# Optimization experiments

Measured on AMD Instinct MI355X. Metric: run time of the kernel, lower is better.

## Reference

```python
import jax, jax.numpy as jnp
import numpy as np

B, D, C, P = 1024, 768, 150, 64  # batch, in_feats, num_labels, proj2 dim
POS_M, NEG_M = 0.7, 1.4


def setup_inputs() -> dict:
    key = jax.random.key(0)
    ks = jax.random.split(key, 8)
    return {
        "x": jax.random.normal(ks[0], (B, D), jnp.float32),
        "lb": jax.random.randint(ks[1], (B,), 0, C + 1),
        "mem": jax.random.normal(ks[2], (C, D), jnp.float32),
        "fc_w": jax.random.normal(ks[3], (2 * D, 2 * D), jnp.float32) * 0.02,
        "fc_b": jnp.zeros((2 * D,), jnp.float32),
        "p1_w": jax.random.normal(ks[4], (1, 2 * D), jnp.float32) * 0.02,
        "p1_b": jnp.zeros((1,), jnp.float32),
        "p2_w": jax.random.normal(ks[5], (P, 2 * D), jnp.float32) * 0.02,
        "p2_b": jnp.zeros((P,), jnp.float32),
    }


def reference(x, lb, mem, fc_w, fc_b, p1_w, p1_b, p2_w, p2_b):
    d = x.shape[1]
    # cat([a, b], 1) @ fc_w.T == a @ Wx.T + b @ Wm.T  (exact split of the linear)
    Wx, Wm = fc_w[:, :d], fc_w[:, d:]
    xh = x @ Wx.T + fc_b                                # [B, 2D]

    # --- get_logit ---
    seen_h = jax.nn.relu(xh[:, None, :] + mem @ Wm.T)   # [B, C, 2D]
    seen = jnp.einsum('bce,e->bc', seen_h, p1_w[0]) + p1_b[0]   # [B, C]
    uh = jax.nn.relu(xh)                                # cat([x, zeros]) path
    unseen = uh @ p1_w.T + p1_b                         # [B, 1]
    logits = jnp.concatenate([seen, unseen], axis=1)    # [B, C+1]

    # --- masked log-softmax losses (pos_adapte) ---
    labels = jax.nn.one_hot(lb, C + 1, dtype=jnp.float32)
    th = jnp.zeros_like(labels).at[:, -1].set(1.0)
    labels = labels.at[:, -1].set(0.0)
    p_mask = labels + th
    n_mask = 1.0 - labels
    BIG = 1e30
    loss1 = -(jax.nn.log_softmax(logits - (1.0 - p_mask) * BIG, -1) * labels).sum(1)
    loss2 = -(jax.nn.log_softmax(logits - (1.0 - n_mask) * BIG, -1) * th).sum(1)
    loss_cls = (loss1 + loss2).mean()

    # --- metric loss on unseen embedding ---
    u = uh @ p2_w.T + p2_b                              # [B, 64]
    u = u / jnp.maximum(jnp.linalg.norm(u, axis=1, keepdims=True), 1e-12)
    sq_n = (u * u).sum(1)
    sq = sq_n[:, None] + sq_n[None, :] - 2.0 * (u @ u.T)
    err = sq <= 0.0
    dist = jnp.sqrt(jnp.clip(sq, 1e-16, None)) * (~err).astype(u.dtype)
    same = lb[:, None] == lb[None, :]
    eye = jnp.eye(dist.shape[0], dtype=bool)
    pos = (same & ~eye).astype(dist.dtype)
    neg = (~same).astype(dist.dtype)
    pos_l = (jax.nn.relu(dist - POS_M) * pos).sum() / jnp.maximum(pos.sum(), 1.0)
    neg_l = (jax.nn.relu(NEG_M - dist) * neg).sum() / jnp.maximum(neg.sum(), 1.0)

    return loss_cls + pos_l + neg_l
```

## Files before the change

kernel.cpp:

```cpp
#include <hip/hip_runtime.h>
#include <math.h>

#define B_    1024
#define D_    768
#define C_    150
#define P_    64
#define TWOD  1536
#define NCLS  151
#define CPAD  256

#define ECHUNKS 16
#define ECHUNK  96
#define ESTEP   32

#define ASTR  40
#define USTRU 120

#define USTR  72

#define OFF_MH      0
#define OFF_XH      (OFF_MH + C_ * TWOD)
#define OFF_PARTIAL (OFF_XH + B_ * TWOD)
#define OFF_UBF     (OFF_PARTIAL + ECHUNKS * B_ * CPAD)
#define OFF_SQN     (OFF_UBF + (B_ * P_) / 2)
#define OFF_CLS     (OFF_SQN + B_)
#define OFF_PAIR    (OFF_CLS + B_)
#define OFF_XBF     (OFF_PAIR + 1024)
#define OFF_MEMBF   (OFF_XBF + (B_ * D_) / 2)
#define OFF_WBF     (OFF_MEMBF + (C_ * D_) / 2)
#define OFF_P2BF    (OFF_WBF + (TWOD * TWOD) / 2)

typedef __bf16 bfx8 __attribute__((ext_vector_type(8)));
typedef float  f32x4 __attribute__((ext_vector_type(4)));

__device__ inline ushort f2bf(float f) {
    union { float f; unsigned u; } c; c.f = f;
    unsigned r = c.u + 0x7fffu + ((c.u >> 16) & 1u);
    return (ushort)(r >> 16);
}

#define X4   (B_ * D_ / 4)
#define MEM4 (C_ * D_ / 4)
#define W4   (TWOD * TWOD / 4)
#define P24  (P_ * TWOD / 4)
#define TOT4 (X4 + MEM4 + W4 + P24)

__global__ __launch_bounds__(256) void prep_bf16(
    const float* __restrict__ x, const float* __restrict__ mem,
    const float* __restrict__ w, const float* __restrict__ p2w,
    ushort* __restrict__ xb, ushort* __restrict__ memb,
    ushort* __restrict__ wb, ushort* __restrict__ p2b)
{
    int i = blockIdx.x * 256 + threadIdx.x;
    if (i >= TOT4) return;
    const float* src; ushort* dst; int off;
    if (i < X4)                  { src = x;   dst = xb;   off = i; }
    else if (i < X4 + MEM4)      { src = mem; dst = memb; off = i - X4; }
    else if (i < X4 + MEM4 + W4) { src = w;   dst = wb;   off = i - X4 - MEM4; }
    else                         { src = p2w; dst = p2b;  off = i - X4 - MEM4 - W4; }
    float4 v = ((const float4*)src)[off];
    ushort4 o;
    o.x = f2bf(v.x); o.y = f2bf(v.y); o.z = f2bf(v.z); o.w = f2bf(v.w);
    ((ushort4*)dst)[off] = o;
}

__global__ __launch_bounds__(256) void gemm_all(
    const ushort* __restrict__ xbf, const ushort* __restrict__ membf,
    const ushort* __restrict__ wbf, const float* __restrict__ fc_b,
    float* __restrict__ xh, float* __restrict__ mh)
{
    __shared__ ushort As[64 * ASTR];
    __shared__ ushort Bs[128 * ASTR];
    const int id = blockIdx.x;
    const int t  = threadIdx.x;

    const ushort* A; float* Out; int M, m0, n0, koff; bool xblk;
    if (id < 192) {
        xblk = true;  A = xbf;  Out = xh; M = B_;
        m0 = (id & 15) * 64; n0 = (id >> 4) * 128; koff = 0;
    } else {
        int q = id - 192;
        xblk = false; A = membf; Out = mh; M = C_;
        m0 = (q % 3) * 64; n0 = (q / 3) * 128; koff = D_;
    }

    const int wave = t >> 6, lane = t & 63;
    const int wm = (wave & 1) * 32, wn = (wave >> 1) * 64;
    const int fm = lane & 15, quad = lane >> 4;

    const int row_a = t >> 2, qa = (t & 3) * 8;
    const int ar = min(m0 + row_a, M - 1);
    const ushort* Arow = A + (size_t)ar * D_ + qa;
    const ushort* Brow = wbf + (size_t)(n0 + row_a) * TWOD + koff + qa;

    f32x4 acc[2][4];
#pragma unroll
    for (int j = 0; j < 4; ++j) {
        float bv = xblk ? fc_b[n0 + wn + j * 16 + fm] : 0.f;
#pragma unroll
        for (int i = 0; i < 2; ++i)
            acc[i][j] = (f32x4){bv, bv, bv, bv};
    }

    uint4 pa  = *(const uint4*)(Arow);
    uint4 pb0 = *(const uint4*)(Brow);
    uint4 pb1 = *(const uint4*)(Brow + 64 * TWOD);

    for (int k0 = 0; k0 < D_; k0 += 32) {
        __syncthreads();
        *(uint4*)&As[row_a * ASTR + qa] = pa;
        *(uint4*)&Bs[row_a * ASTR + qa] = pb0;
        *(uint4*)&Bs[(64 + row_a) * ASTR + qa] = pb1;
        __syncthreads();
        if (k0 + 32 < D_) {
            pa  = *(const uint4*)(Arow + k0 + 32);
            pb0 = *(const uint4*)(Brow + k0 + 32);
            pb1 = *(const uint4*)(Brow + 64 * TWOD + k0 + 32);
        }
        bfx8 af[2], bf[4];
#pragma unroll
        for (int i = 0; i < 2; ++i)
            af[i] = *(const bfx8*)&As[(wm + i * 16 + fm) * ASTR + quad * 8];
#pragma unroll
        for (int j = 0; j < 4; ++j)
            bf[j] = *(const bfx8*)&Bs[(wn + j * 16 + fm) * ASTR + quad * 8];
#pragma unroll
        for (int i = 0; i < 2; ++i)
#pragma unroll
            for (int j = 0; j < 4; ++j)
                acc[i][j] = __builtin_amdgcn_mfma_f32_16x16x32_bf16(
                    af[i], bf[j], acc[i][j], 0, 0, 0);
    }

#pragma unroll
    for (int i = 0; i < 2; ++i)
#pragma unroll
        for (int j = 0; j < 4; ++j)
#pragma unroll
            for (int r = 0; r < 4; ++r) {
                int row = m0 + wm + i * 16 + quad * 4 + r;
                int col = n0 + wn + j * 16 + fm;
                if (row < M) Out[(size_t)row * TWOD + col] = acc[i][j][r];
            }
}

__global__ __launch_bounds__(256) void fused_tile(
    const float* __restrict__ xh, const float* __restrict__ mh,
    const float* __restrict__ p1w, const ushort* __restrict__ p2bf,
    float* __restrict__ partial)
{
    __shared__ __align__(16) char smem[46080];
    const int t  = threadIdx.x;
    const int b0 = blockIdx.x * 128;
    const int z  = blockIdx.z;

    if (blockIdx.y == 3) {
        ushort* Au = (ushort*)smem;
        ushort* Wu = (ushort*)(smem + 128 * USTRU * 2);
        const int kb = z * ECHUNK;
        const int wave = t >> 6, lane = t & 63;
        const int fm = lane & 15, quad = lane >> 4;

        {
            const int row = t >> 1, kh = (t & 1) * 48;
            const float* xr_ = xh + (size_t)(b0 + row) * TWOD + kb + kh;
            ushort tmp[48];
#pragma unroll
            for (int i = 0; i < 12; ++i) {
                float4 v = *(const float4*)&xr_[i * 4];
                tmp[i * 4 + 0] = f2bf(fmaxf(v.x, 0.f));
                tmp[i * 4 + 1] = f2bf(fmaxf(v.y, 0.f));
                tmp[i * 4 + 2] = f2bf(fmaxf(v.z, 0.f));
                tmp[i * 4 + 3] = f2bf(fmaxf(v.w, 0.f));
            }
#pragma unroll
            for (int i = 0; i < 6; ++i)
                *(uint4*)&Au[row * USTRU + kh + i * 8] = *(const uint4*)&tmp[i * 8];
        }
        {
            const int row = t >> 2, ks = (t & 3) * 24;
            const ushort* pw = p2bf + (size_t)row * TWOD + kb + ks;
#pragma unroll
            for (int i = 0; i < 3; ++i)
                *(uint4*)&Wu[row * USTRU + ks + i * 8] = *(const uint4*)&pw[i * 8];
        }
        __syncthreads();

        f32x4 uacc[2][4];
#pragma unroll
        for (int i = 0; i < 2; ++i)
#pragma unroll
            for (int j = 0; j < 4; ++j) uacc[i][j] = (f32x4){0.f, 0.f, 0.f, 0.f};
#pragma unroll
        for (int k0 = 0; k0 < ECHUNK; k0 += 32) {
            bfx8 af[2], bf[4];
#pragma unroll
            for (int i = 0; i < 2; ++i)
                af[i] = *(const bfx8*)&Au[(wave * 32 + i * 16 + fm) * USTRU + k0 + quad * 8];
#pragma unroll
            for (int j = 0; j < 4; ++j)
                bf[j] = *(const bfx8*)&Wu[(j * 16 + fm) * USTRU + k0 + quad * 8];
#pragma unroll
            for (int i = 0; i < 2; ++i)
#pragma unroll
                for (int j = 0; j < 4; ++j)
                    uacc[i][j] = __builtin_amdgcn_mfma_f32_16x16x32_bf16(
                        af[i], bf[j], uacc[i][j], 0, 0, 0);
        }
#pragma unroll
        for (int i = 0; i < 2; ++i)
#pragma unroll
            for (int j = 0; j < 4; ++j)
#pragma unroll
                for (int r = 0; r < 4; ++r) {
                    int row = b0 + wave * 32 + i * 16 + quad * 4 + r;
                    partial[((size_t)z * B_ + row) * CPAD + 192 + j * 16 + fm] =
                        uacc[i][j][r];
                }
        return;
    }

    float* xT  = (float*)smem;
    float* mT  = (float*)(smem + ESTEP * 128 * 4);
    float* wT1 = (float*)(smem + ESTEP * 192 * 4);

    const int c0 = blockIdx.y * 64;
    const int e0 = z * ECHUNK;
    const int tm = t & 15;
    const int tn = t >> 4;

    const int xr = t & 127, xh16 = (t >> 7) * 16;
    const int mc = t & 63,  mq8 = ((t >> 6) & 3) * 8;
    const int gc = c0 + mc;
    const bool cseen = gc < C_;
    const float* xrow = xh + (size_t)(b0 + xr) * TWOD;
    const float* mrow = mh + (size_t)(cseen ? gc : 0) * TWOD;

    float acc[8][4] = {};

    for (int es = 0; es < ECHUNK; es += ESTEP) {
        const int eb = e0 + es;
        float4 xv[4];
#pragma unroll
        for (int i = 0; i < 4; ++i)
            xv[i] = *(const float4*)&xrow[eb + xh16 + i * 4];
        float4 mv0 = cseen ? *(const float4*)&mrow[eb + mq8]
                           : make_float4(0.f, 0.f, 0.f, 0.f);
        float4 mv1 = cseen ? *(const float4*)&mrow[eb + mq8 + 4]
                           : make_float4(0.f, 0.f, 0.f, 0.f);
        float4 wv = (t < 8) ? *(const float4*)&p1w[eb + t * 4]
                            : make_float4(0.f, 0.f, 0.f, 0.f);
        __syncthreads();
#pragma unroll
        for (int i = 0; i < 4; ++i) {
            xT[(xh16 + i * 4 + 0) * 128 + xr] = xv[i].x;
            xT[(xh16 + i * 4 + 1) * 128 + xr] = xv[i].y;
            xT[(xh16 + i * 4 + 2) * 128 + xr] = xv[i].z;
            xT[(xh16 + i * 4 + 3) * 128 + xr] = xv[i].w;
        }
        mT[(mq8 + 0) * 64 + mc] = mv0.x; mT[(mq8 + 1) * 64 + mc] = mv0.y;
        mT[(mq8 + 2) * 64 + mc] = mv0.z; mT[(mq8 + 3) * 64 + mc] = mv0.w;
        mT[(mq8 + 4) * 64 + mc] = mv1.x; mT[(mq8 + 5) * 64 + mc] = mv1.y;
        mT[(mq8 + 6) * 64 + mc] = mv1.z; mT[(mq8 + 7) * 64 + mc] = mv1.w;
        if (t < 8) *(float4*)&wT1[t * 4] = wv;
        __syncthreads();

#pragma unroll 4
        for (int e = 0; e < ESTEP; ++e) {
            float a[8], m[4];
            *(float4*)&a[0] = *(const float4*)&xT[e * 128 + tm * 8];
            *(float4*)&a[4] = *(const float4*)&xT[e * 128 + tm * 8 + 4];
            *(float4*)&m[0] = *(const float4*)&mT[e * 64 + tn * 4];
            const float w = wT1[e];
#pragma unroll
            for (int i = 0; i < 8; ++i)
#pragma unroll
                for (int j = 0; j < 4; ++j)
                    acc[i][j] = fmaf(fmaxf(a[i] + m[j], 0.f), w, acc[i][j]);
        }
    }

#pragma unroll
    for (int i = 0; i < 8; ++i) {
        const int gb = b0 + tm * 8 + i;
        float4 v = make_float4(acc[i][0], acc[i][1], acc[i][2], acc[i][3]);
        *(float4*)&partial[((size_t)z * B_ + gb) * CPAD + c0 + tn * 4] = v;
    }
}

__global__ __launch_bounds__(256) void reduce_row(
    const float* __restrict__ partial,
    const float* __restrict__ p1b, const float* __restrict__ p2b,
    const int* __restrict__ lb,
    ushort* __restrict__ ubf, float* __restrict__ sqn,
    float* __restrict__ clsbuf)
{
    const int b = blockIdx.x, t = threadIdx.x;
    float v = 0.f;
#pragma unroll
    for (int z = 0; z < ECHUNKS; ++z)
        v += partial[((size_t)z * B_ + b) * CPAD + t];
    if (t < NCLS)       v += p1b[0];
    else if (t >= 192)  v += p2b[t - 192];

    __shared__ float sval[256];
    sval[t] = v;
    __syncthreads();

    if (t < 64) {
        float uv = sval[192 + t];
        float s = uv * uv;
#pragma unroll
        for (int off = 32; off; off >>= 1) s += __shfl_xor(s, off);
        float inv = 1.f / fmaxf(sqrtf(s), 1e-12f);
        ubf[(size_t)b * P_ + t] = f2bf(uv * inv);
        if (t == 0) sqn[b] = s * inv * inv;

        const int l = lb[b];
        float mx = -1e30f;
        for (int j = t; j < NCLS; j += 64)
            if (!(j == l && l < C_)) mx = fmaxf(mx, sval[j]);
#pragma unroll
        for (int off = 32; off; off >>= 1) mx = fmaxf(mx, __shfl_xor(mx, off));
        float se = 0.f;
        for (int j = t; j < NCLS; j += 64)
            if (!(j == l && l < C_)) se += expf(sval[j] - mx);
#pragma unroll
        for (int off = 32; off; off >>= 1) se += __shfl_xor(se, off);

        if (t == 0) {
            float l150  = sval[C_];
            float loss2 = mx + logf(se) - l150;
            float loss1 = 0.f;
            if (l < C_) {
                float a  = sval[l];
                float m2 = fmaxf(a, l150);
                loss1 = m2 - a + logf(expf(a - m2) + expf(l150 - m2));
            }
            clsbuf[b] = loss1 + loss2;
        }
    }
}

__global__ __launch_bounds__(256) void pair_loss(
    const ushort* __restrict__ ubf, const float* __restrict__ sqn,
    const int* __restrict__ lb, float* __restrict__ pairpart)
{
    __shared__ ushort ui_s[64 * USTR];
    __shared__ ushort uj_s[64 * USTR];
    __shared__ float sni[64], snj[64];
    __shared__ int   li[64],  lj[64];
    __shared__ float red[4][4];

    const int t  = threadIdx.x;
    const int i0 = blockIdx.x * 64, j0 = blockIdx.y * 64;

    for (int idx = t; idx < 512; idx += 256) {
        int row = idx >> 3, ch = (idx & 7) * 8;
        *(uint4*)&ui_s[row * USTR + ch] =
            *(const uint4*)&ubf[(size_t)(i0 + row) * P_ + ch];
        *(uint4*)&uj_s[row * USTR + ch] =
            *(const uint4*)&ubf[(size_t)(j0 + row) * P_ + ch];
    }
    if (t < 64)       { sni[t] = sqn[i0 + t]; li[t] = lb[i0 + t]; }
    else if (t < 128) { int q = t - 64; snj[q] = sqn[j0 + q]; lj[q] = lb[j0 + q]; }
    __syncthreads();

    const int wave = t >> 6, lane = t & 63;
    const int n = lane & 15, quad = lane >> 4;
    const int iw = wave * 16;

    const bfx8 af0 = *(const bfx8*)&ui_s[(iw + n) * USTR + quad * 8];
    const bfx8 af1 = *(const bfx8*)&ui_s[(iw + n) * USTR + quad * 8 + 32];

    f32x4 acc[4];
#pragma unroll
    for (int jt = 0; jt < 4; ++jt) {
        const bfx8 bf0 = *(const bfx8*)&uj_s[(jt * 16 + n) * USTR + quad * 8];
        const bfx8 bf1 = *(const bfx8*)&uj_s[(jt * 16 + n) * USTR + quad * 8 + 32];
        acc[jt] = __builtin_amdgcn_mfma_f32_16x16x32_bf16(
            af0, bf0, (f32x4){0.f, 0.f, 0.f, 0.f}, 0, 0, 0);
        acc[jt] = __builtin_amdgcn_mfma_f32_16x16x32_bf16(
            af1, bf1, acc[jt], 0, 0, 0);
    }

    float ps = 0.f, pc = 0.f, ns = 0.f, nc = 0.f;
#pragma unroll
    for (int jt = 0; jt < 4; ++jt)
#pragma unroll
        for (int r = 0; r < 4; ++r) {
            const int il = iw + quad * 4 + r;
            const int jl = jt * 16 + n;
            float sq = sni[il] + snj[jl] - 2.f * acc[jt][r];
            float dist = sq > 0.f ? sqrtf(fmaxf(sq, 1e-16f)) : 0.f;
            bool same = (li[il] == lj[jl]);
            if (same) {
                if (i0 + il != j0 + jl) { ps += fmaxf(dist - 0.7f, 0.f); pc += 1.f; }
            } else {
                ns += fmaxf(1.4f - dist, 0.f); nc += 1.f;
            }
        }

#pragma unroll
    for (int off = 32; off; off >>= 1) {
        ps += __shfl_xor(ps, off); pc += __shfl_xor(pc, off);
        ns += __shfl_xor(ns, off); nc += __shfl_xor(nc, off);
    }
    if (lane == 0) { red[0][wave] = ps; red[1][wave] = pc;
                     red[2][wave] = ns; red[3][wave] = nc; }
    __syncthreads();
    if (t == 0) {
        float4 v;
        v.x = red[0][0] + red[0][1] + red[0][2] + red[0][3];
        v.y = red[1][0] + red[1][1] + red[1][2] + red[1][3];
        v.z = red[2][0] + red[2][1] + red[2][2] + red[2][3];
        v.w = red[3][0] + red[3][1] + red[3][2] + red[3][3];
        *(float4*)&pairpart[(size_t)(blockIdx.y * 16 + blockIdx.x) * 4] = v;
    }
}

__global__ __launch_bounds__(256) void finalize(
    const float* __restrict__ clsbuf, const float* __restrict__ pairpart,
    float* __restrict__ out)
{
    __shared__ float red[5][4];
    const int t = threadIdx.x;
    float c = clsbuf[t] + clsbuf[t + 256] + clsbuf[t + 512] + clsbuf[t + 768];
    float4 pp = *(const float4*)&pairpart[(size_t)t * 4];
    float ps = pp.x, pc = pp.y, ns = pp.z, nc = pp.w;
#pragma unroll
    for (int off = 32; off; off >>= 1) {
        c  += __shfl_xor(c, off);
        ps += __shfl_xor(ps, off); pc += __shfl_xor(pc, off);
        ns += __shfl_xor(ns, off); nc += __shfl_xor(nc, off);
    }
    const int wave = t >> 6, lane = t & 63;
    if (lane == 0) { red[0][wave] = c; red[1][wave] = ps; red[2][wave] = pc;
                     red[3][wave] = ns; red[4][wave] = nc; }
    __syncthreads();
    if (t == 0) {
        float C = 0.f, PS = 0.f, PC = 0.f, NS = 0.f, NC = 0.f;
#pragma unroll
        for (int w = 0; w < 4; ++w) {
            C += red[0][w]; PS += red[1][w]; PC += red[2][w];
            NS += red[3][w]; NC += red[4][w];
        }
        out[0] = C / (float)B_ + PS / fmaxf(PC, 1.f) + NS / fmaxf(NC, 1.f);
    }
}

extern "C" void kernel_launch(void* const* d_in, const int* in_sizes, int n_in,
                              void* d_out, int out_size, void* d_ws, size_t ws_size,
                              hipStream_t stream)
{
    const float* x    = (const float*)d_in[0];
    const int*   lb   = (const int*)d_in[1];
    const float* mem  = (const float*)d_in[2];
    const float* fc_w = (const float*)d_in[3];
    const float* fc_b = (const float*)d_in[4];
    const float* p1w  = (const float*)d_in[5];
    const float* p1b  = (const float*)d_in[6];
    const float* p2w  = (const float*)d_in[7];
    const float* p2b  = (const float*)d_in[8];

    float* ws       = (float*)d_ws;
    float* mh       = ws + OFF_MH;
    float* xh       = ws + OFF_XH;
    float* partials = ws + OFF_PARTIAL;
    ushort* ubf     = (ushort*)(ws + OFF_UBF);
    float* sqn      = ws + OFF_SQN;
    float* clsbuf   = ws + OFF_CLS;
    float* pairpart = ws + OFF_PAIR;
    ushort* xbf     = (ushort*)(ws + OFF_XBF);
    ushort* membf   = (ushort*)(ws + OFF_MEMBF);
    ushort* wbf     = (ushort*)(ws + OFF_WBF);
    ushort* p2bf    = (ushort*)(ws + OFF_P2BF);

    prep_bf16<<<(TOT4 + 255) / 256, 256, 0, stream>>>(x, mem, fc_w, p2w,
                                                      xbf, membf, wbf, p2bf);
    gemm_all<<<228, 256, 0, stream>>>(xbf, membf, wbf, fc_b, xh, mh);
    fused_tile<<<dim3(8, 4, ECHUNKS), 256, 0, stream>>>(xh, mh, p1w, p2bf,
                                                        partials);
    reduce_row<<<B_, 256, 0, stream>>>(partials, p1b, p2b, lb, ubf, sqn, clsbuf);
    pair_loss<<<dim3(16, 16), 256, 0, stream>>>(ubf, sqn, lb, pairpart);
    finalize<<<1, 256, 0, stream>>>(clsbuf, pairpart, (float*)d_out);
}
```

Baseline: 143.9 us.

## Store xh/mh in fp16 and use packed half add-relu-dot2 in seen-logit tile

The GEMM now writes xh and mh as fp16 instead of fp32, which halves the intermediate traffic. The main fused tile computes relu(x+m)·w with packed half2 adds, half2 max and fdot2 into fp32 accumulators, staging a whole 96-wide chunk once rather than looping with syncs. The p1/p2 weights and the unseen/pairwise MFMA paths switch from bf16 to fp16. This trades fp32 accuracy in the B×C×2D elementwise stage for roughly double ALU throughput. It also risks fp16 rounding error in the sum and relu before the dot.

```diff
diff --git a/kernel.cpp b/kernel.cpp
--- a/kernel.cpp
+++ b/kernel.cpp
@@ -11,70 +11,96 @@
 
 #define ECHUNKS 16
 #define ECHUNK  96
-#define ESTEP   32
 
 #define ASTR  40
 #define USTRU 120
-
 #define USTR  72
 
 #define OFF_MH      0
-#define OFF_XH      (OFF_MH + C_ * TWOD)
-#define OFF_PARTIAL (OFF_XH + B_ * TWOD)
-#define OFF_UBF     (OFF_PARTIAL + ECHUNKS * B_ * CPAD)
-#define OFF_SQN     (OFF_UBF + (B_ * P_) / 2)
+#define OFF_XH      (OFF_MH + (C_ * TWOD) / 2)
+#define OFF_PARTIAL (OFF_XH + (B_ * TWOD) / 2)
+#define OFF_UHF     (OFF_PARTIAL + ECHUNKS * B_ * CPAD)
+#define OFF_SQN     (OFF_UHF + (B_ * P_) / 2)
 #define OFF_CLS     (OFF_SQN + B_)
 #define OFF_PAIR    (OFF_CLS + B_)
 #define OFF_XBF     (OFF_PAIR + 1024)
 #define OFF_MEMBF   (OFF_XBF + (B_ * D_) / 2)
 #define OFF_WBF     (OFF_MEMBF + (C_ * D_) / 2)
-#define OFF_P2BF    (OFF_WBF + (TWOD * TWOD) / 2)
-
-typedef __bf16 bfx8 __attribute__((ext_vector_type(8)));
-typedef float  f32x4 __attribute__((ext_vector_type(4)));
+#define OFF_P2H     (OFF_WBF + (TWOD * TWOD) / 2)
+#define OFF_P1H     (OFF_P2H + (P_ * TWOD) / 2)
+
+typedef __bf16    bfx8   __attribute__((ext_vector_type(8)));
+typedef _Float16  fp16x8 __attribute__((ext_vector_type(8)));
+typedef _Float16  h2v    __attribute__((ext_vector_type(2)));
+typedef float     f32x4  __attribute__((ext_vector_type(4)));
 
 __device__ inline ushort f2bf(float f) {
     union { float f; unsigned u; } c; c.f = f;
     unsigned r = c.u + 0x7fffu + ((c.u >> 16) & 1u);
     return (ushort)(r >> 16);
 }
+__device__ inline ushort f2h(float f) {
+    _Float16 h = (_Float16)f;
+    return __builtin_bit_cast(ushort, h);
+}
+__device__ inline unsigned addrelu2(unsigned a, unsigned m) {
+    h2v s = __builtin_bit_cast(h2v, a) + __builtin_bit_cast(h2v, m);
+    h2v z = {(_Float16)0.f, (_Float16)0.f};
+    s = __builtin_elementwise_max(s, z);
+    return __builtin_bit_cast(unsigned, s);
+}
+__device__ inline unsigned relu2(unsigned a) {
+    h2v s = __builtin_bit_cast(h2v, a);
+    h2v z = {(_Float16)0.f, (_Float16)0.f};
+    s = __builtin_elementwise_max(s, z);
+    return __builtin_bit_cast(unsigned, s);
+}
+__device__ inline float dot2acc(unsigned a, unsigned b, float c) {
+    return __builtin_amdgcn_fdot2(__builtin_bit_cast(h2v, a),
+                                  __builtin_bit_cast(h2v, b), c, false);
+}
 
 #define X4   (B_ * D_ / 4)
 #define MEM4 (C_ * D_ / 4)
 #define W4   (TWOD * TWOD / 4)
 #define P24  (P_ * TWOD / 4)
-#define TOT4 (X4 + MEM4 + W4 + P24)
-
-__global__ __launch_bounds__(256) void prep_bf16(
+#define P14  (TWOD / 4)
+#define TOT4 (X4 + MEM4 + W4 + P24 + P14)
+
+__global__ __launch_bounds__(256) void prep_cvt(
     const float* __restrict__ x, const float* __restrict__ mem,
     const float* __restrict__ w, const float* __restrict__ p2w,
+    const float* __restrict__ p1w,
     ushort* __restrict__ xb, ushort* __restrict__ memb,
-    ushort* __restrict__ wb, ushort* __restrict__ p2b)
+    ushort* __restrict__ wb, ushort* __restrict__ p2h,
+    ushort* __restrict__ p1h)
 {
     int i = blockIdx.x * 256 + threadIdx.x;
     if (i >= TOT4) return;
-    const float* src; ushort* dst; int off;
-    if (i < X4)                  { src = x;   dst = xb;   off = i; }
-    else if (i < X4 + MEM4)      { src = mem; dst = memb; off = i - X4; }
-    else if (i < X4 + MEM4 + W4) { src = w;   dst = wb;   off = i - X4 - MEM4; }
-    else                         { src = p2w; dst = p2b;  off = i - X4 - MEM4 - W4; }
+    const float* src; ushort* dst; int off; bool bf;
+    if (i < X4)                        { src = x;   dst = xb;   off = i; bf = true; }
+    else if (i < X4 + MEM4)            { src = mem; dst = memb; off = i - X4; bf = true; }
+    else if (i < X4 + MEM4 + W4)       { src = w;   dst = wb;   off = i - X4 - MEM4; bf = true; }
+    else if (i < X4 + MEM4 + W4 + P24) { src = p2w; dst = p2h;  off = i - X4 - MEM4 - W4; bf = false; }
+    else                               { src = p1w; dst = p1h;  off = i - X4 - MEM4 - W4 - P24; bf = false; }
     float4 v = ((const float4*)src)[off];
     ushort4 o;
-    o.x = f2bf(v.x); o.y = f2bf(v.y); o.z = f2bf(v.z); o.w = f2bf(v.w);
+    if (bf) { o.x = f2bf(v.x); o.y = f2bf(v.y); o.z = f2bf(v.z); o.w = f2bf(v.w); }
+    else    { o.x = f2h(v.x);  o.y = f2h(v.y);  o.z = f2h(v.z);  o.w = f2h(v.w); }
     ((ushort4*)dst)[off] = o;
 }
 
 __global__ __launch_bounds__(256) void gemm_all(
     const ushort* __restrict__ xbf, const ushort* __restrict__ membf,
     const ushort* __restrict__ wbf, const float* __restrict__ fc_b,
-    float* __restrict__ xh, float* __restrict__ mh)
+    ushort* __restrict__ xh, ushort* __restrict__ mh)
 {
     __shared__ ushort As[64 * ASTR];
     __shared__ ushort Bs[128 * ASTR];
     const int id = blockIdx.x;
     const int t  = threadIdx.x;
 
-    const ushort* A; float* Out; int M, m0, n0, koff; bool xblk;
+    const ushort* A; ushort* Out; int M, m0, n0, koff; bool xblk;
     if (id < 192) {
         xblk = true;  A = xbf;  Out = xh; M = B_;
         m0 = (id & 15) * 64; n0 = (id >> 4) * 128; koff = 0;
@@ -140,46 +166,43 @@
             for (int r = 0; r < 4; ++r) {
                 int row = m0 + wm + i * 16 + quad * 4 + r;
                 int col = n0 + wn + j * 16 + fm;
-                if (row < M) Out[(size_t)row * TWOD + col] = acc[i][j][r];
+                if (row < M) Out[(size_t)row * TWOD + col] = f2h(acc[i][j][r]);
             }
 }
 
 __global__ __launch_bounds__(256) void fused_tile(
-    const float* __restrict__ xh, const float* __restrict__ mh,
-    const float* __restrict__ p1w, const ushort* __restrict__ p2bf,
+    const ushort* __restrict__ xh, const ushort* __restrict__ mh,
+    const ushort* __restrict__ p1h, const ushort* __restrict__ p2h,
     float* __restrict__ partial)
 {
     __shared__ __align__(16) char smem[46080];
     const int t  = threadIdx.x;
     const int b0 = blockIdx.x * 128;
     const int z  = blockIdx.z;
+    const int e0 = z * ECHUNK;
 
     if (blockIdx.y == 3) {
         ushort* Au = (ushort*)smem;
-        ushort* Wu = (ushort*)(smem + 128 * USTRU * 2);
-        const int kb = z * ECHUNK;
+        ushort* Wu = (ushort*)(smem + 30720);
         const int wave = t >> 6, lane = t & 63;
         const int fm = lane & 15, quad = lane >> 4;
 
         {
             const int row = t >> 1, kh = (t & 1) * 48;
-            const float* xr_ = xh + (size_t)(b0 + row) * TWOD + kb + kh;
-            ushort tmp[48];
-#pragma unroll
-            for (int i = 0; i < 12; ++i) {
-                float4 v = *(const float4*)&xr_[i * 4];
-                tmp[i * 4 + 0] = f2bf(fmaxf(v.x, 0.f));
-                tmp[i * 4 + 1] = f2bf(fmaxf(v.y, 0.f));
-                tmp[i * 4 + 2] = f2bf(fmaxf(v.z, 0.f));
-                tmp[i * 4 + 3] = f2bf(fmaxf(v.w, 0.f));
+            const ushort* src = xh + (size_t)(b0 + row) * TWOD + e0 + kh;
+            uint4 v[6];
+#pragma unroll
+            for (int i = 0; i < 6; ++i) v[i] = *(const uint4*)&src[i * 8];
+#pragma unroll
+            for (int i = 0; i < 6; ++i) {
+                v[i].x = relu2(v[i].x); v[i].y = relu2(v[i].y);
+                v[i].z = relu2(v[i].z); v[i].w = relu2(v[i].w);
+                *(uint4*)&Au[row * USTRU + kh + i * 8] = v[i];
             }
-#pragma unroll
-            for (int i = 0; i < 6; ++i)
-                *(uint4*)&Au[row * USTRU + kh + i * 8] = *(const uint4*)&tmp[i * 8];
         }
         {
             const int row = t >> 2, ks = (t & 3) * 24;
-            const ushort* pw = p2bf + (size_t)row * TWOD + kb + ks;
+            const ushort* pw = p2h + (size_t)row * TWOD + e0 + ks;
 #pragma unroll
             for (int i = 0; i < 3; ++i)
                 *(uint4*)&Wu[row * USTRU + ks + i * 8] = *(const uint4*)&pw[i * 8];
@@ -193,18 +216,18 @@
             for (int j = 0; j < 4; ++j) uacc[i][j] = (f32x4){0.f, 0.f, 0.f, 0.f};
 #pragma unroll
         for (int k0 = 0; k0 < ECHUNK; k0 += 32) {
-            bfx8 af[2], bf[4];
+            fp16x8 af[2], bf[4];
 #pragma unroll
             for (int i = 0; i < 2; ++i)
-                af[i] = *(const bfx8*)&Au[(wave * 32 + i * 16 + fm) * USTRU + k0 + quad * 8];
+                af[i] = *(const fp16x8*)&Au[(wave * 32 + i * 16 + fm) * USTRU + k0 + quad * 8];
 #pragma unroll
             for (int j = 0; j < 4; ++j)
-                bf[j] = *(const bfx8*)&Wu[(j * 16 + fm) * USTRU + k0 + quad * 8];
+                bf[j] = *(const fp16x8*)&Wu[(j * 16 + fm) * USTRU + k0 + quad * 8];
 #pragma unroll
             for (int i = 0; i < 2; ++i)
 #pragma unroll
                 for (int j = 0; j < 4; ++j)
-                    uacc[i][j] = __builtin_amdgcn_mfma_f32_16x16x32_bf16(
+                    uacc[i][j] = __builtin_amdgcn_mfma_f32_16x16x32_f16(
                         af[i], bf[j], uacc[i][j], 0, 0, 0);
         }
 #pragma unroll
@@ -220,64 +243,69 @@
         return;
     }
 
-    float* xT  = (float*)smem;
-    float* mT  = (float*)(smem + ESTEP * 128 * 4);
-    float* wT1 = (float*)(smem + ESTEP * 192 * 4);
-
+    unsigned* xT = (unsigned*)smem;
+    unsigned* mT = (unsigned*)(smem + 24576);
+    unsigned* wT = (unsigned*)(smem + 36864);
     const int c0 = blockIdx.y * 64;
-    const int e0 = z * ECHUNK;
-    const int tm = t & 15;
-    const int tn = t >> 4;
-
-    const int xr = t & 127, xh16 = (t >> 7) * 16;
-    const int mc = t & 63,  mq8 = ((t >> 6) & 3) * 8;
-    const int gc = c0 + mc;
-    const bool cseen = gc < C_;
-    const float* xrow = xh + (size_t)(b0 + xr) * TWOD;
-    const float* mrow = mh + (size_t)(cseen ? gc : 0) * TWOD;
+    const int tm = t & 15, tn = t >> 4;
+
+    {
+        const int row = t >> 1, ph = (t & 1) * 48;
+        const ushort* src = xh + (size_t)(b0 + row) * TWOD + e0 + ph;
+        uint4 v[6];
+#pragma unroll
+        for (int i = 0; i < 6; ++i) v[i] = *(const uint4*)&src[i * 8];
+#pragma unroll
+        for (int i = 0; i < 6; ++i) {
+            const int ep = (t & 1) * 24 + i * 4;
+            xT[(ep + 0) * 128 + row] = v[i].x;
+            xT[(ep + 1) * 128 + row] = v[i].y;
+            xT[(ep + 2) * 128 + row] = v[i].z;
+            xT[(ep + 3) * 128 + row] = v[i].w;
+        }
+    }
+    {
+        const int col = t & 63, seg = t >> 6;
+        const int gc  = c0 + col;
+        uint4 v[3];
+        if (gc < C_) {
+            const ushort* src = mh + (size_t)gc * TWOD + e0 + seg * 24;
+#pragma unroll
+            for (int i = 0; i < 3; ++i) v[i] = *(const uint4*)&src[i * 8];
+        } else {
+#pragma unroll
+            for (int i = 0; i < 3; ++i) v[i] = make_uint4(0, 0, 0, 0);
+        }
+#pragma unroll
+        for (int i = 0; i < 3; ++i) {
+            const int ep = seg * 12 + i * 4;
+            mT[(ep + 0) * 64 + col] = v[i].x;
+            mT[(ep + 1) * 64 + col] = v[i].y;
+            mT[(ep + 2) * 64 + col] = v[i].z;
+            mT[(ep + 3) * 64 + col] = v[i].w;
+        }
+    }
+    if (t < 12) {
+        uint4 v = *(const uint4*)&p1h[e0 + t * 8];
+        wT[t * 4 + 0] = v.x; wT[t * 4 + 1] = v.y;
+        wT[t * 4 + 2] = v.z; wT[t * 4 + 3] = v.w;
+    }
+    __syncthreads();
 
     float acc[8][4] = {};
-
-    for (int es = 0; es < ECHUNK; es += ESTEP) {
-        const int eb = e0 + es;
-        float4 xv[4];
-#pragma unroll
-        for (int i = 0; i < 4; ++i)
-            xv[i] = *(const float4*)&xrow[eb + xh16 + i * 4];
-        float4 mv0 = cseen ? *(const float4*)&mrow[eb + mq8]
-                           : make_float4(0.f, 0.f, 0.f, 0.f);
-        float4 mv1 = cseen ? *(const float4*)&mrow[eb + mq8 + 4]
-                           : make_float4(0.f, 0.f, 0.f, 0.f);
-        float4 wv = (t < 8) ? *(const float4*)&p1w[eb + t * 4]
-                            : make_float4(0.f, 0.f, 0.f, 0.f);
-        __syncthreads();
-#pragma unroll
-        for (int i = 0; i < 4; ++i) {
-            xT[(xh16 + i * 4 + 0) * 128 + xr] = xv[i].x;
-            xT[(xh16 + i * 4 + 1) * 128 + xr] = xv[i].y;
-            xT[(xh16 + i * 4 + 2) * 128 + xr] = xv[i].z;
-            xT[(xh16 + i * 4 + 3) * 128 + xr] = xv[i].w;
-        }
-        mT[(mq8 + 0) * 64 + mc] = mv0.x; mT[(mq8 + 1) * 64 + mc] = mv0.y;
-        mT[(mq8 + 2) * 64 + mc] = mv0.z; mT[(mq8 + 3) * 64 + mc] = mv0.w;
-        mT[(mq8 + 4) * 64 + mc] = mv1.x; mT[(mq8 + 5) * 64 + mc] = mv1.y;
-        mT[(mq8 + 6) * 64 + mc] = mv1.z; mT[(mq8 + 7) * 64 + mc] = mv1.w;
-        if (t < 8) *(float4*)&wT1[t * 4] = wv;
-        __syncthreads();
-
 #pragma unroll 4
-        for (int e = 0; e < ESTEP; ++e) {
-            float a[8], m[4];
-            *(float4*)&a[0] = *(const float4*)&xT[e * 128 + tm * 8];
-            *(float4*)&a[4] = *(const float4*)&xT[e * 128 + tm * 8 + 4];
-            *(float4*)&m[0] = *(const float4*)&mT[e * 64 + tn * 4];
-            const float w = wT1[e];
-#pragma unroll
-            for (int i = 0; i < 8; ++i)
-#pragma unroll
-                for (int j = 0; j < 4; ++j)
-                    acc[i][j] = fmaf(fmaxf(a[i] + m[j], 0.f), w, acc[i][j]);
-        }
+    for (int ep = 0; ep < 48; ++ep) {
+        uint4 a0 = *(const uint4*)&xT[ep * 128 + tm * 8];
+        uint4 a1 = *(const uint4*)&xT[ep * 128 + tm * 8 + 4];
+        uint4 mj = *(const uint4*)&mT[ep * 64 + tn * 4];
+        const unsigned wv = wT[ep];
+        const unsigned aa[8] = {a0.x, a0.y, a0.z, a0.w, a1.x, a1.y, a1.z, a1.w};
+        const unsigned mm[4] = {mj.x, mj.y, mj.z, mj.w};
+#pragma unroll
+        for (int i = 0; i < 8; ++i)
+#pragma unroll
+            for (int j = 0; j < 4; ++j)
+                acc[i][j] = dot2acc(addrelu2(aa[i], mm[j]), wv, acc[i][j]);
     }
 
 #pragma unroll
@@ -292,7 +320,7 @@
     const float* __restrict__ partial,
     const float* __restrict__ p1b, const float* __restrict__ p2b,
     const int* __restrict__ lb,
-    ushort* __restrict__ ubf, float* __restrict__ sqn,
+    ushort* __restrict__ uhf, float* __restrict__ sqn,
     float* __restrict__ clsbuf)
 {
     const int b = blockIdx.x, t = threadIdx.x;
@@ -313,7 +341,7 @@
 #pragma unroll
         for (int off = 32; off; off >>= 1) s += __shfl_xor(s, off);
         float inv = 1.f / fmaxf(sqrtf(s), 1e-12f);
-        ubf[(size_t)b * P_ + t] = f2bf(uv * inv);
+        uhf[(size_t)b * P_ + t] = f2h(uv * inv);
         if (t == 0) sqn[b] = s * inv * inv;
 
         const int l = lb[b];
@@ -343,7 +371,7 @@
 }
 
 __global__ __launch_bounds__(256) void pair_loss(
-    const ushort* __restrict__ ubf, const float* __restrict__ sqn,
+    const ushort* __restrict__ uhf, const float* __restrict__ sqn,
     const int* __restrict__ lb, float* __restrict__ pairpart)
 {
     __shared__ ushort ui_s[64 * USTR];
@@ -358,9 +386,9 @@
     for (int idx = t; idx < 512; idx += 256) {
         int row = idx >> 3, ch = (idx & 7) * 8;
         *(uint4*)&ui_s[row * USTR + ch] =
-            *(const uint4*)&ubf[(size_t)(i0 + row) * P_ + ch];
+            *(const uint4*)&uhf[(size_t)(i0 + row) * P_ + ch];
         *(uint4*)&uj_s[row * USTR + ch] =
-            *(const uint4*)&ubf[(size_t)(j0 + row) * P_ + ch];
+            *(const uint4*)&uhf[(size_t)(j0 + row) * P_ + ch];
     }
     if (t < 64)       { sni[t] = sqn[i0 + t]; li[t] = lb[i0 + t]; }
     else if (t < 128) { int q = t - 64; snj[q] = sqn[j0 + q]; lj[q] = lb[j0 + q]; }
@@ -370,17 +398,17 @@
     const int n = lane & 15, quad = lane >> 4;
     const int iw = wave * 16;
 
-    const bfx8 af0 = *(const bfx8*)&ui_s[(iw + n) * USTR + quad * 8];
-    const bfx8 af1 = *(const bfx8*)&ui_s[(iw + n) * USTR + quad * 8 + 32];
+    const fp16x8 af0 = *(const fp16x8*)&ui_s[(iw + n) * USTR + quad * 8];
+    const fp16x8 af1 = *(const fp16x8*)&ui_s[(iw + n) * USTR + quad * 8 + 32];
 
     f32x4 acc[4];
 #pragma unroll
     for (int jt = 0; jt < 4; ++jt) {
-        const bfx8 bf0 = *(const bfx8*)&uj_s[(jt * 16 + n) * USTR + quad * 8];
-        const bfx8 bf1 = *(const bfx8*)&uj_s[(jt * 16 + n) * USTR + quad * 8 + 32];
-        acc[jt] = __builtin_amdgcn_mfma_f32_16x16x32_bf16(
+        const fp16x8 bf0 = *(const fp16x8*)&uj_s[(jt * 16 + n) * USTR + quad * 8];
+        const fp16x8 bf1 = *(const fp16x8*)&uj_s[(jt * 16 + n) * USTR + quad * 8 + 32];
+        acc[jt] = __builtin_amdgcn_mfma_f32_16x16x32_f16(
             af0, bf0, (f32x4){0.f, 0.f, 0.f, 0.f}, 0, 0, 0);
-        acc[jt] = __builtin_amdgcn_mfma_f32_16x16x32_bf16(
+        acc[jt] = __builtin_amdgcn_mfma_f32_16x16x32_f16(
             af1, bf1, acc[jt], 0, 0, 0);
     }
 
@@ -464,24 +492,25 @@
     const float* p2b  = (const float*)d_in[8];
 
     float* ws       = (float*)d_ws;
-    float* mh       = ws + OFF_MH;
-    float* xh       = ws + OFF_XH;
+    ushort* mh      = (ushort*)(ws + OFF_MH);
+    ushort* xh      = (ushort*)(ws + OFF_XH);
     float* partials = ws + OFF_PARTIAL;
-    ushort* ubf     = (ushort*)(ws + OFF_UBF);
+    ushort* uhf     = (ushort*)(ws + OFF_UHF);
     float* sqn      = ws + OFF_SQN;
     float* clsbuf   = ws + OFF_CLS;
     float* pairpart = ws + OFF_PAIR;
     ushort* xbf     = (ushort*)(ws + OFF_XBF);
     ushort* membf   = (ushort*)(ws + OFF_MEMBF);
     ushort* wbf     = (ushort*)(ws + OFF_WBF);
-    ushort* p2bf    = (ushort*)(ws + OFF_P2BF);
-
-    prep_bf16<<<(TOT4 + 255) / 256, 256, 0, stream>>>(x, mem, fc_w, p2w,
-                                                      xbf, membf, wbf, p2bf);
+    ushort* p2h     = (ushort*)(ws + OFF_P2H);
+    ushort* p1h     = (ushort*)(ws + OFF_P1H);
+
+    prep_cvt<<<(TOT4 + 255) / 256, 256, 0, stream>>>(x, mem, fc_w, p2w, p1w,
+                                                     xbf, membf, wbf, p2h, p1h);
     gemm_all<<<228, 256, 0, stream>>>(xbf, membf, wbf, fc_b, xh, mh);
-    fused_tile<<<dim3(8, 4, ECHUNKS), 256, 0, stream>>>(xh, mh, p1w, p2bf,
+    fused_tile<<<dim3(8, 4, ECHUNKS), 256, 0, stream>>>(xh, mh, p1h, p2h,
                                                         partials);
-    reduce_row<<<B_, 256, 0, stream>>>(partials, p1b, p2b, lb, ubf, sqn, clsbuf);
-    pair_loss<<<dim3(16, 16), 256, 0, stream>>>(ubf, sqn, lb, pairpart);
+    reduce_row<<<B_, 256, 0, stream>>>(partials, p1b, p2b, lb, uhf, sqn, clsbuf);
+    pair_loss<<<dim3(16, 16), 256, 0, stream>>>(uhf, sqn, lb, pairpart);
     finalize<<<1, 256, 0, stream>>>(clsbuf, pairpart, (float*)d_out);
 }
```

Measured after the change: 132.2 us. -8.2%, faster.
